# Kernel tuning notes

Measured on AMD Instinct MI355X. Metric: run time of the kernel, lower is better.

Reference implementation:

```python
import jax, jax.numpy as jnp
import numpy as np

DT = 1e-3
MAX_UPDATE = 0.1


def setup_inputs() -> dict:
    key = jax.random.key(0)
    k1, k2 = jax.random.split(key)
    B, T = 512, 8192
    inputs = jax.random.normal(k1, (B, T, 2), dtype=jnp.float32)
    # learned 2x2 kernel, keras 'uniform' init ~ U(-0.05, 0.05)
    A = jax.random.uniform(k2, (2, 2), dtype=jnp.float32, minval=-0.05, maxval=0.05)
    # physical model coefficients (from coeffs tuple)
    C = jnp.eye(2, dtype=jnp.float32)
    D = 1e-3 * jnp.eye(2, dtype=jnp.float32)
    return {"inputs": inputs, "A": A, "C": C, "D": D}


def reference(inputs, A, C, D):
    # inputs: [B, T, 2] measurement increments dy
    B = inputs.shape[0]
    # initial state per GRNNmodel.initial_state: x0=[1,0], cov0=eye(2)
    x0 = jnp.tile(jnp.array([[1.0, 0.0]], dtype=inputs.dtype), (B, 1))      # [B,2]
    cov0 = jnp.tile(jnp.eye(2, dtype=inputs.dtype)[None], (B, 1, 1))        # [B,2,2]

    Ct = C.T
    Dt = D.T

    def step(carry, dy):
        x, cov = carry                                   # [B,2], [B,2,2]
        out = jnp.einsum('ij,bj->bi', C, x) * DT         # output uses pre-update state
        xicov = cov @ Ct + Dt                            # [B,2,2]
        A_minus_xiC = A - xicov @ C                      # [B,2,2]
        dx = jnp.einsum('bij,bj->bi', A_minus_xiC, x) * DT \
             + jnp.einsum('bij,bj->bi', xicov, dy)
        x_new = x + jnp.clip(dx, -MAX_UPDATE, MAX_UPDATE)
        cov_dt = (jnp.einsum('ij,bjk->bik', A, cov)
                  + jnp.einsum('bij,kj->bik', cov, A)    # cov @ A^T
                  + D
                  - xicov @ jnp.swapaxes(xicov, 1, 2))
        cov_new = jnp.clip(cov + cov_dt * DT, -1.0, 1.0)
        return (x_new, cov_new), out

    dys = jnp.swapaxes(inputs, 0, 1)                     # [T,B,2]
    _, outs = jax.lax.scan(step, (x0, cov0), dys)
    return jnp.swapaxes(outs, 0, 1)                      # [B,T,2]
```

## Files before the change

### kernel.cpp

```cpp
#include <hip/hip_runtime.h>


#define DT_C 1e-3f
#define MAXU 0.1f
#define T_LEN 8192
#define T4 (T_LEN / 2)
#define CHUNK 256
#define G_CHUNK (CHUNK / 2)
#define NCHUNK (T_LEN / CHUNK)
#define BROWS 512

__device__ __forceinline__ float clipf(float v, float lo, float hi) {
    return fminf(fmaxf(v, lo), hi);
}
#define MEDU(x) __builtin_amdgcn_fmed3f((x), -MAXU, MAXU)
#define SB() __builtin_amdgcn_sched_barrier(0)

__global__ __launch_bounds__(256) void transpose_f4(
    const float4* __restrict__ src, float4* __restrict__ dst,
    int rows, int cols)
{
    __shared__ float4 tile[32][33];
    const int tx = threadIdx.x & 31;
    const int ty = threadIdx.x >> 5;
    const int c0 = blockIdx.x * 32;
    const int r0 = blockIdx.y * 32;
#pragma unroll
    for (int i = 0; i < 32; i += 8)
        tile[ty + i][tx] = src[(size_t)(r0 + ty + i) * cols + (c0 + tx)];
    __syncthreads();
#pragma unroll
    for (int i = 0; i < 32; i += 8)
        dst[(size_t)(c0 + ty + i) * rows + (r0 + tx)] = tile[tx][ty + i];
}

__global__ __launch_bounds__(128, 1) void grnn_fused2(
    const float4* __restrict__ inT, const float* __restrict__ Am,
    const float* __restrict__ Cm, const float* __restrict__ Dm,
    float4* __restrict__ outT)
{
    __shared__ float4 wlds[2][CHUNK * 2];
    __shared__ float4 sbnd[CHUNK / 8];
    const int tid = threadIdx.x;
    const int wv = tid >> 6;

    if (wv == 1) {
        const int lane = tid & 63;
        const float a00 = Am[0], a01 = Am[1], a10 = Am[2], a11 = Am[3];
        const float c00 = Cm[0], c01 = Cm[1], c10 = Cm[2], c11 = Cm[3];
        const float d00 = Dm[0], d01 = Dm[1], d10 = Dm[2], d11 = Dm[3];
        const bool special = (c00 == 1.f) && (c01 == 0.f) && (c10 == 0.f) &&
                             (c11 == 1.f) && (d01 == 0.f) && (d10 == 0.f);
        const float adt00 = a00 * DT_C, adt01 = a01 * DT_C;
        const float adt10 = a10 * DT_C, adt11 = a11 * DT_C;

        if (special) {
            const float K00 = 1.f + 2.f * adt00, A2dt01 = 2.f * adt01;
            const float K11 = 1.f + 2.f * adt11, A2dt10 = 2.f * adt10;
            const float K01 = 1.f + (a00 + a11) * DT_C;
            const float C0u = DT_C * d00 * (1.f - 2.f * a00);
            const float C0v = DT_C * d11 * (1.f - 2.f * a11);
            const float C1w = -(adt10 * d00 + adt01 * d11);

#define XSTEP()                                                               \
            {                                                                 \
                const float w2 = w * w;                                       \
                const float gu = fmaf(-DT_C, u, K00);                         \
                const float gv = fmaf(-DT_C, v, K11);                         \
                const float s  = u + v;                                       \
                const float ru = fmaf(A2dt01, w, fmaf(-DT_C, w2, C0u));       \
                const float rv = fmaf(A2dt10, w, fmaf(-DT_C, w2, C0v));       \
                const float gw = fmaf(-DT_C, s, K01);                         \
                const float rw = fmaf(adt10, u, fmaf(adt01, v, C1w));         \
                const float un = fmaf(u, gu, ru);                             \
                const float vn = fmaf(v, gv, rv);                             \
                const float wn = fmaf(w, gw, rw);                             \
                u = un; v = vn; w = wn;                                       \
            }

            float u = 1.f + d00, w = 0.f, v = 1.f + d11;
            for (int it = 0; it <= NCHUNK; ++it) {
                if (it < NCHUNK) {
                    if (lane == 0) {
                        for (int j = 0; j < CHUNK / 8; ++j) {
                            sbnd[j] = make_float4(u, w, v, 0.f);
                            XSTEP() XSTEP() XSTEP() XSTEP()
                            XSTEP() XSTEP() XSTEP() XSTEP()
                        }
                    }
                    asm volatile("s_waitcnt lgkmcnt(0)" ::: "memory");
                    SB();
                    __builtin_amdgcn_wave_barrier();
                    if (lane < CHUNK / 8) {
                        const float4 sb = sbnd[lane];
                        float u2 = sb.x, w2v = sb.y, v2 = sb.z;
                        float4* wdst = wlds[it & 1] + 2 * (lane * 8);
#pragma unroll
                        for (int k = 0; k < 8; ++k) {
                            float4 mv, xv;
                            mv.x = fmaf(-DT_C, u2, adt00);
                            mv.y = fmaf(-DT_C, w2v, adt10);
                            mv.z = fmaf(-DT_C, w2v, adt01);
                            mv.w = fmaf(-DT_C, v2, adt11);
                            xv = make_float4(u2, w2v, w2v, v2);
                            wdst[2 * k]     = mv;
                            wdst[2 * k + 1] = xv;
                            {
                                float u = u2, w = w2v, v = v2;
                                XSTEP()
                                u2 = u; w2v = w; v2 = v;
                            }
                        }
                    }
                }
                __syncthreads();
            }
#undef XSTEP
        } else {
#define RSTEP_G()                                                             \
            {                                                                 \
                const float xi00 = p00*c00 + p01*c01 + d00;                   \
                const float xi01 = p00*c10 + p01*c11 + d10;                   \
                const float xi10 = p10*c00 + p11*c01 + d01;                   \
                const float xi11 = p10*c10 + p11*c11 + d11;                   \
                const float g00 = a00*p00 + a01*p10 + p00*a00 + p01*a01 + d00 - (xi00*xi00 + xi01*xi01); \
                const float g01 = a00*p01 + a01*p11 + p00*a10 + p01*a11 + d01 - (xi00*xi10 + xi01*xi11); \
                const float g10 = a10*p00 + a11*p10 + p10*a00 + p11*a01 + d10 - (xi10*xi00 + xi11*xi01); \
                const float g11 = a10*p01 + a11*p11 + p10*a10 + p11*a11 + d11 - (xi10*xi10 + xi11*xi11); \
                p00 = clipf(p00 + g00 * DT_C, -1.f, 1.f);                     \
                p01 = clipf(p01 + g01 * DT_C, -1.f, 1.f);                     \
                p10 = clipf(p10 + g10 * DT_C, -1.f, 1.f);                     \
                p11 = clipf(p11 + g11 * DT_C, -1.f, 1.f);                     \
            }
            float p00 = 1.f, p01 = 0.f, p10 = 0.f, p11 = 1.f;
            for (int it = 0; it <= NCHUNK; ++it) {
                if (it < NCHUNK) {
                    if (lane == 0) {
                        for (int j = 0; j < CHUNK / 8; ++j) {
                            sbnd[j] = make_float4(p00, p01, p10, p11);
                            RSTEP_G() RSTEP_G() RSTEP_G() RSTEP_G()
                            RSTEP_G() RSTEP_G() RSTEP_G() RSTEP_G()
                        }
                    }
                    asm volatile("s_waitcnt lgkmcnt(0)" ::: "memory");
                    SB();
                    __builtin_amdgcn_wave_barrier();
                    if (lane < CHUNK / 8) {
                        const float4 sb = sbnd[lane];
                        float p00 = sb.x, p01 = sb.y, p10 = sb.z, p11 = sb.w;
                        float4* wdst = wlds[it & 1] + 2 * (lane * 8);
#pragma unroll
                        for (int k = 0; k < 8; ++k) {
                            const float xi00 = p00*c00 + p01*c01 + d00;
                            const float xi01 = p00*c10 + p01*c11 + d10;
                            const float xi10 = p10*c00 + p11*c01 + d01;
                            const float xi11 = p10*c10 + p11*c11 + d11;
                            const float m00 = a00 - (xi00*c00 + xi01*c10);
                            const float m01 = a01 - (xi00*c01 + xi01*c11);
                            const float m10 = a10 - (xi10*c00 + xi11*c10);
                            const float m11 = a11 - (xi10*c01 + xi11*c11);
                            float4 mv, xv;
                            mv.x = m00 * DT_C; mv.y = m10 * DT_C;
                            mv.z = m01 * DT_C; mv.w = m11 * DT_C;
                            xv = make_float4(xi00, xi10, xi01, xi11);
                            wdst[2 * k]     = mv;
                            wdst[2 * k + 1] = xv;
                            RSTEP_G()
                        }
                    }
                }
                __syncthreads();
            }
#undef RSTEP_G
        }
    } else {
        const int lane = tid;
        const int b = blockIdx.x * 64 + lane;
        const float cdt00 = Cm[0] * DT_C, cdt01 = Cm[1] * DT_C;
        const float cdt10 = Cm[2] * DT_C, cdt11 = Cm[3] * DT_C;
        float x0 = 1.f, x1 = 0.f;

#define IDX(G) ((size_t)(G) * BROWS + b)

        float4 d0 = inT[IDX(0)], d1 = inT[IDX(1)], d2 = inT[IDX(2)], d3 = inT[IDX(3)];
        float4 d4 = inT[IDX(4)], d5 = inT[IDX(5)], d6 = inT[IDX(6)], d7 = inT[IDX(7)];
        float4 s0a, s0b, s0c, s0d, s1a, s1b, s1c, s1d;
        float4 t0a, t0b, t0c, t0d, t1a, t1b, t1c, t1d;

#define WLG(P, G)                                                             \
        {                                                                     \
            const int gg = (G) < G_CHUNK ? (G) : (G_CHUNK - 1);               \
            const float4* wp = wbuf + 4 * gg;                                 \
            P##a = wp[0]; P##b = wp[1]; P##c = wp[2]; P##d = wp[3];           \
        }

#define GRANC(P, DJ, OG)                                                      \
        {                                                                     \
            const float4 dyv = DJ;                                            \
            {                                                                 \
                const int nog = (OG) + 8;                                     \
                const int rg = nog < T4 ? nog : (T4 - 1);                     \
                DJ = inT[IDX(rg)];                                            \
            }                                                                 \
            float4 ov;                                                        \
            ov.x = fmaf(cdt00, x0, cdt01 * x1);                               \
            ov.y = fmaf(cdt10, x0, cdt11 * x1);                               \
            float e0 = fmaf(P##b.x, dyv.x, P##b.z * dyv.y);                   \
            float e1 = fmaf(P##b.y, dyv.x, P##b.w * dyv.y);                   \
            float dx0 = fmaf(P##a.x, x0, fmaf(P##a.z, x1, e0));               \
            float dx1 = fmaf(P##a.y, x0, fmaf(P##a.w, x1, e1));               \
            x0 += MEDU(dx0);                                                  \
            x1 += MEDU(dx1);                                                  \
            ov.z = fmaf(cdt00, x0, cdt01 * x1);                               \
            ov.w = fmaf(cdt10, x0, cdt11 * x1);                               \
            e0 = fmaf(P##d.x, dyv.z, P##d.z * dyv.w);                         \
            e1 = fmaf(P##d.y, dyv.z, P##d.w * dyv.w);                         \
            dx0 = fmaf(P##c.x, x0, fmaf(P##c.z, x1, e0));                     \
            dx1 = fmaf(P##c.y, x0, fmaf(P##c.w, x1, e1));                     \
            x0 += MEDU(dx0);                                                  \
            x1 += MEDU(dx1);                                                  \
            outT[IDX(OG)] = ov;                                               \
        }

        for (int it = 0; it <= NCHUNK; ++it) {
            if (it > 0) {
                const int cc = it - 1;
                const float4* wbuf = wlds[cc & 1];
                const int ogc = cc * G_CHUNK;
                WLG(s0, 0) WLG(s1, 1) WLG(t0, 2) WLG(t1, 3)
                SB();
                for (int q = 0; q < G_CHUNK / 8; ++q) {
                    const int g = 8 * q;
                    const int og = ogc + g;
                    GRANC(s0, d0, og + 0) GRANC(s1, d1, og + 1) SB();
                    WLG(s0, g + 4) WLG(s1, g + 5) SB();
                    GRANC(t0, d2, og + 2) GRANC(t1, d3, og + 3) SB();
                    WLG(t0, g + 6) WLG(t1, g + 7) SB();
                    GRANC(s0, d4, og + 4) GRANC(s1, d5, og + 5) SB();
                    WLG(s0, g + 8) WLG(s1, g + 9) SB();
                    GRANC(t0, d6, og + 6) GRANC(t1, d7, og + 7) SB();
                    WLG(t0, g + 10) WLG(t1, g + 11) SB();
                }
            }
            __syncthreads();
        }
#undef GRANC
#undef WLG
#undef IDX
    }
}

__global__ __launch_bounds__(64) void grnn_mono(
    const float* __restrict__ inp, const float* __restrict__ Am,
    const float* __restrict__ Cm, const float* __restrict__ Dm,
    float* __restrict__ out, int B)
{
    const int b = blockIdx.x * blockDim.x + threadIdx.x;
    if (b >= B) return;
    const float a00 = Am[0], a01 = Am[1], a10 = Am[2], a11 = Am[3];
    const float c00 = Cm[0], c01 = Cm[1], c10 = Cm[2], c11 = Cm[3];
    const float d00 = Dm[0], d01 = Dm[1], d10 = Dm[2], d11 = Dm[3];
    float x0 = 1.0f, x1 = 0.0f;
    float p00 = 1.0f, p01 = 0.0f, p10 = 0.0f, p11 = 1.0f;
    const float2* __restrict__ in2 = reinterpret_cast<const float2*>(inp) + (size_t)b * T_LEN;
    float2* __restrict__ out2 = reinterpret_cast<float2*>(out) + (size_t)b * T_LEN;
#pragma unroll 4
    for (int t = 0; t < T_LEN; ++t) {
        float2 o;
        o.x = (c00 * x0 + c01 * x1) * DT_C;
        o.y = (c10 * x0 + c11 * x1) * DT_C;
        out2[t] = o;
        const float xi00 = p00 * c00 + p01 * c01 + d00;
        const float xi01 = p00 * c10 + p01 * c11 + d10;
        const float xi10 = p10 * c00 + p11 * c01 + d01;
        const float xi11 = p10 * c10 + p11 * c11 + d11;
        const float m00 = a00 - (xi00 * c00 + xi01 * c10);
        const float m01 = a01 - (xi00 * c01 + xi01 * c11);
        const float m10 = a10 - (xi10 * c00 + xi11 * c10);
        const float m11 = a11 - (xi10 * c01 + xi11 * c11);
        const float2 dy = in2[t];
        float dx0 = (m00 * x0 + m01 * x1) * DT_C + xi00 * dy.x + xi01 * dy.y;
        float dx1 = (m10 * x0 + m11 * x1) * DT_C + xi10 * dy.x + xi11 * dy.y;
        x0 += clipf(dx0, -MAXU, MAXU);
        x1 += clipf(dx1, -MAXU, MAXU);
        const float g00 = a00*p00 + a01*p10 + p00*a00 + p01*a01 + d00 - (xi00*xi00 + xi01*xi01);
        const float g01 = a00*p01 + a01*p11 + p00*a10 + p01*a11 + d01 - (xi00*xi10 + xi01*xi11);
        const float g10 = a10*p00 + a11*p10 + p10*a00 + p11*a01 + d10 - (xi10*xi00 + xi11*xi01);
        const float g11 = a10*p01 + a11*p11 + p10*a10 + p11*a11 + d11 - (xi10*xi10 + xi11*xi11);
        p00 = clipf(p00 + g00 * DT_C, -1.0f, 1.0f);
        p01 = clipf(p01 + g01 * DT_C, -1.0f, 1.0f);
        p10 = clipf(p10 + g10 * DT_C, -1.0f, 1.0f);
        p11 = clipf(p11 + g11 * DT_C, -1.0f, 1.0f);
    }
}

extern "C" void kernel_launch(void* const* d_in, const int* in_sizes, int n_in,
                              void* d_out, int out_size, void* d_ws, size_t ws_size,
                              hipStream_t stream) {
    const float* inp = (const float*)d_in[0];
    const float* Am  = (const float*)d_in[1];
    const float* Cm  = (const float*)d_in[2];
    const float* Dm  = (const float*)d_in[3];
    float* out = (float*)d_out;
    const int B = in_sizes[0] / (T_LEN * 2);

    float4* inT  = (float4*)d_ws;
    float4* outT = inT + (size_t)T4 * BROWS;
    const size_t need_ws = (size_t)2 * T4 * BROWS * sizeof(float4);

    if (B == BROWS && d_ws != nullptr && ws_size >= need_ws) {
        hipLaunchKernelGGL(transpose_f4, dim3(T4 / 32, BROWS / 32), dim3(256),
                           0, stream,
                           reinterpret_cast<const float4*>(inp), inT,
                           BROWS, T4);
        hipLaunchKernelGGL(grnn_fused2, dim3(BROWS / 64), dim3(128), 0,
                           stream, inT, Am, Cm, Dm, outT);
        hipLaunchKernelGGL(transpose_f4, dim3(BROWS / 32, T4 / 32), dim3(256),
                           0, stream,
                           outT, reinterpret_cast<float4*>(out), T4, BROWS);
    } else {
        hipLaunchKernelGGL(grnn_mono, dim3((B + 63) / 64), dim3(64), 0, stream,
                           inp, Am, Cm, Dm, out, B);
    }
}
```

Measured before the change: 514.0 us.

## Process two batch rows per lane with packed FP32 math, halving block count

The consumer wave now handles two batch rows per lane (b0 and b0+64) and does the per-step state update with 2-wide vector FMA and min/max, which lets the compiler emit packed FP32 instructions. The grid shrinks from 8 to 4 blocks, so the covariance/gain recurrence wave's work is shared across twice as many rows. The aim is to amortise the serial covariance computation and raise ILP by interleaving two independent recurrences. The cost is fewer blocks on the GPU, which lengthens the critical path if the covariance producer wave is the bottleneck, plus higher register pressure.

```diff
diff --git a/kernel.cpp b/kernel.cpp
--- a/kernel.cpp
+++ b/kernel.cpp
@@ -10,10 +10,19 @@
 #define NCHUNK (T_LEN / CHUNK)
 #define BROWS 512
 
+typedef float f2 __attribute__((ext_vector_type(2)));
+typedef float f4v __attribute__((ext_vector_type(4)));
+
 __device__ __forceinline__ float clipf(float v, float lo, float hi) {
     return fminf(fmaxf(v, lo), hi);
 }
-#define MEDU(x) __builtin_amdgcn_fmed3f((x), -MAXU, MAXU)
+__device__ __forceinline__ f2 pkfma(f2 a, f2 b, f2 c) {
+    return __builtin_elementwise_fma(a, b, c);
+}
+__device__ __forceinline__ f2 pkclip(f2 v) {
+    const f2 lo = {-MAXU, -MAXU}, hi = {MAXU, MAXU};
+    return __builtin_elementwise_min(__builtin_elementwise_max(v, lo), hi);
+}
 #define SB() __builtin_amdgcn_sched_barrier(0)
 
 __global__ __launch_bounds__(256) void transpose_f4(
@@ -34,7 +43,7 @@
         dst[(size_t)(c0 + ty + i) * rows + (r0 + tx)] = tile[tx][ty + i];
 }
 
-__global__ __launch_bounds__(128, 1) void grnn_fused2(
+__global__ __launch_bounds__(128, 1) void grnn_fused3(
     const float4* __restrict__ inT, const float* __restrict__ Am,
     const float* __restrict__ Cm, const float* __restrict__ Dm,
     float4* __restrict__ outT)
@@ -175,51 +184,62 @@
         }
     } else {
         const int lane = tid;
-        const int b = blockIdx.x * 64 + lane;
-        const float cdt00 = Cm[0] * DT_C, cdt01 = Cm[1] * DT_C;
-        const float cdt10 = Cm[2] * DT_C, cdt11 = Cm[3] * DT_C;
-        float x0 = 1.f, x1 = 0.f;
-
-#define IDX(G) ((size_t)(G) * BROWS + b)
-
-        float4 d0 = inT[IDX(0)], d1 = inT[IDX(1)], d2 = inT[IDX(2)], d3 = inT[IDX(3)];
-        float4 d4 = inT[IDX(4)], d5 = inT[IDX(5)], d6 = inT[IDX(6)], d7 = inT[IDX(7)];
-        float4 s0a, s0b, s0c, s0d, s1a, s1b, s1c, s1d;
-        float4 t0a, t0b, t0c, t0d, t1a, t1b, t1c, t1d;
+        const int b0 = blockIdx.x * 128 + lane;
+        const int b1 = b0 + 64;
+        const f2 CC0 = {Cm[0] * DT_C, Cm[2] * DT_C};
+        const f2 CC1 = {Cm[1] * DT_C, Cm[3] * DT_C};
+        const f4v* __restrict__ inTv = reinterpret_cast<const f4v*>(inT);
+        f4v* __restrict__ outTv = reinterpret_cast<f4v*>(outT);
+
+        f2 XA = {1.f, 0.f}, XB = {1.f, 0.f};
+        f4v dA0 = inTv[(size_t)0 * BROWS + b0], dB0 = inTv[(size_t)0 * BROWS + b1];
+        f4v dA1 = inTv[(size_t)1 * BROWS + b0], dB1 = inTv[(size_t)1 * BROWS + b1];
+        f4v dA2 = inTv[(size_t)2 * BROWS + b0], dB2 = inTv[(size_t)2 * BROWS + b1];
+        f4v dA3 = inTv[(size_t)3 * BROWS + b0], dB3 = inTv[(size_t)3 * BROWS + b1];
+        f4v dA4 = inTv[(size_t)4 * BROWS + b0], dB4 = inTv[(size_t)4 * BROWS + b1];
+        f4v dA5 = inTv[(size_t)5 * BROWS + b0], dB5 = inTv[(size_t)5 * BROWS + b1];
+        f4v dA6 = inTv[(size_t)6 * BROWS + b0], dB6 = inTv[(size_t)6 * BROWS + b1];
+        f4v dA7 = inTv[(size_t)7 * BROWS + b0], dB7 = inTv[(size_t)7 * BROWS + b1];
+        f4v s0a, s0b, s0c, s0d, s1a, s1b, s1c, s1d;
+        f4v t0a, t0b, t0c, t0d, t1a, t1b, t1c, t1d;
 
 #define WLG(P, G)                                                             \
         {                                                                     \
             const int gg = (G) < G_CHUNK ? (G) : (G_CHUNK - 1);               \
-            const float4* wp = wbuf + 4 * gg;                                 \
+            const f4v* wp = reinterpret_cast<const f4v*>(wbuf + 4 * gg);      \
             P##a = wp[0]; P##b = wp[1]; P##c = wp[2]; P##d = wp[3];           \
         }
 
-#define GRANC(P, DJ, OG)                                                      \
+#define GRAN2(P, DA, DB, OG)                                                  \
         {                                                                     \
-            const float4 dyv = DJ;                                            \
+            const f4v yA = DA, yB = DB;                                       \
             {                                                                 \
                 const int nog = (OG) + 8;                                     \
                 const int rg = nog < T4 ? nog : (T4 - 1);                     \
-                DJ = inT[IDX(rg)];                                            \
+                DA = inTv[(size_t)rg * BROWS + b0];                           \
+                DB = inTv[(size_t)rg * BROWS + b1];                           \
             }                                                                 \
-            float4 ov;                                                        \
-            ov.x = fmaf(cdt00, x0, cdt01 * x1);                               \
-            ov.y = fmaf(cdt10, x0, cdt11 * x1);                               \
-            float e0 = fmaf(P##b.x, dyv.x, P##b.z * dyv.y);                   \
-            float e1 = fmaf(P##b.y, dyv.x, P##b.w * dyv.y);                   \
-            float dx0 = fmaf(P##a.x, x0, fmaf(P##a.z, x1, e0));               \
-            float dx1 = fmaf(P##a.y, x0, fmaf(P##a.w, x1, e1));               \
-            x0 += MEDU(dx0);                                                  \
-            x1 += MEDU(dx1);                                                  \
-            ov.z = fmaf(cdt00, x0, cdt01 * x1);                               \
-            ov.w = fmaf(cdt10, x0, cdt11 * x1);                               \
-            e0 = fmaf(P##d.x, dyv.z, P##d.z * dyv.w);                         \
-            e1 = fmaf(P##d.y, dyv.z, P##d.w * dyv.w);                         \
-            dx0 = fmaf(P##c.x, x0, fmaf(P##c.z, x1, e0));                     \
-            dx1 = fmaf(P##c.y, x0, fmaf(P##c.w, x1, e1));                     \
-            x0 += MEDU(dx0);                                                  \
-            x1 += MEDU(dx1);                                                  \
-            outT[IDX(OG)] = ov;                                               \
+            const f2 ma0 = P##a.xy, ma1 = P##a.zw;                            \
+            const f2 xb0 = P##b.xy, xb1 = P##b.zw;                            \
+            const f2 mc0 = P##c.xy, mc1 = P##c.zw;                            \
+            const f2 xd0 = P##d.xy, xd1 = P##d.zw;                            \
+            const f2 oA0 = pkfma(CC1, XA.yy, CC0 * XA.xx);                    \
+            const f2 oB0 = pkfma(CC1, XB.yy, CC0 * XB.xx);                    \
+            const f2 eA0 = pkfma(xb1, yA.yy, xb0 * yA.xx);                    \
+            const f2 eB0 = pkfma(xb1, yB.yy, xb0 * yB.xx);                    \
+            XA += pkclip(pkfma(ma0, XA.xx, pkfma(ma1, XA.yy, eA0)));          \
+            XB += pkclip(pkfma(ma0, XB.xx, pkfma(ma1, XB.yy, eB0)));          \
+            const f2 oA1 = pkfma(CC1, XA.yy, CC0 * XA.xx);                    \
+            const f2 oB1 = pkfma(CC1, XB.yy, CC0 * XB.xx);                    \
+            const f2 eA1 = pkfma(xd1, yA.ww, xd0 * yA.zz);                    \
+            const f2 eB1 = pkfma(xd1, yB.ww, xd0 * yB.zz);                    \
+            XA += pkclip(pkfma(mc0, XA.xx, pkfma(mc1, XA.yy, eA1)));          \
+            XB += pkclip(pkfma(mc0, XB.xx, pkfma(mc1, XB.yy, eB1)));          \
+            f4v o4A, o4B;                                                     \
+            o4A.xy = oA0; o4A.zw = oA1;                                       \
+            o4B.xy = oB0; o4B.zw = oB1;                                       \
+            outTv[(size_t)(OG) * BROWS + b0] = o4A;                           \
+            outTv[(size_t)(OG) * BROWS + b1] = o4B;                           \
         }
 
         for (int it = 0; it <= NCHUNK; ++it) {
@@ -232,21 +252,20 @@
                 for (int q = 0; q < G_CHUNK / 8; ++q) {
                     const int g = 8 * q;
                     const int og = ogc + g;
-                    GRANC(s0, d0, og + 0) GRANC(s1, d1, og + 1) SB();
+                    GRAN2(s0, dA0, dB0, og + 0) GRAN2(s1, dA1, dB1, og + 1) SB();
                     WLG(s0, g + 4) WLG(s1, g + 5) SB();
-                    GRANC(t0, d2, og + 2) GRANC(t1, d3, og + 3) SB();
+                    GRAN2(t0, dA2, dB2, og + 2) GRAN2(t1, dA3, dB3, og + 3) SB();
                     WLG(t0, g + 6) WLG(t1, g + 7) SB();
-                    GRANC(s0, d4, og + 4) GRANC(s1, d5, og + 5) SB();
+                    GRAN2(s0, dA4, dB4, og + 4) GRAN2(s1, dA5, dB5, og + 5) SB();
                     WLG(s0, g + 8) WLG(s1, g + 9) SB();
-                    GRANC(t0, d6, og + 6) GRANC(t1, d7, og + 7) SB();
+                    GRAN2(t0, dA6, dB6, og + 6) GRAN2(t1, dA7, dB7, og + 7) SB();
                     WLG(t0, g + 10) WLG(t1, g + 11) SB();
                 }
             }
             __syncthreads();
         }
-#undef GRANC
+#undef GRAN2
 #undef WLG
-#undef IDX
     }
 }
 
@@ -313,7 +332,7 @@
                            0, stream,
                            reinterpret_cast<const float4*>(inp), inT,
                            BROWS, T4);
-        hipLaunchKernelGGL(grnn_fused2, dim3(BROWS / 64), dim3(128), 0,
+        hipLaunchKernelGGL(grnn_fused3, dim3(BROWS / 128), dim3(128), 0,
                            stream, inT, Am, Cm, Dm, outT);
         hipLaunchKernelGGL(transpose_f4, dim3(BROWS / 32, T4 / 32), dim3(256),
                            0, stream,
```

Result: slower. 711.7 us (+38.5%).
